# Performance work log

Hardware: AMD Instinct MI355X
Metric: run time of the kernel (lower is better)

## Reference

```python
import jax, jax.numpy as jnp
import numpy as np

N_NODES = 100000
N_EDGES = 1600000
IN_F = 128
HID = 128
N_ACT = 32
N_GRAPHS = 256


def setup_inputs() -> dict:
    key = jax.random.key(0)
    ks = jax.random.split(key, 8)
    x = jax.random.normal(ks[0], (N_NODES, IN_F), dtype=jnp.float32)
    edge_index = jax.random.randint(ks[1], (2, N_EDGES), 0, N_NODES, dtype=jnp.int64 if jax.config.read('jax_enable_x64') else jnp.int32)
    batch = jnp.sort(jax.random.randint(ks[2], (N_NODES,), 0, N_GRAPHS))
    def glorot(k, shape):
        fan_in = shape[0]
        return jax.random.normal(k, shape, dtype=jnp.float32) / jnp.sqrt(jnp.float32(fan_in))
    return {
        'x': x,
        'edge_index': edge_index,
        'batch': batch,
        'W1': glorot(ks[3], (IN_F, HID)), 'b1': jnp.zeros((HID,), jnp.float32),
        'W2': glorot(ks[4], (HID, HID)), 'b2': jnp.zeros((HID,), jnp.float32),
        'Wl1': glorot(ks[5], (HID, HID)), 'bl1': jnp.zeros((HID,), jnp.float32),
        'Wl2': glorot(ks[6], (HID, N_ACT)), 'bl2': jnp.zeros((N_ACT,), jnp.float32),
    }


def gcn_conv(x, src, dst, W, b, n_nodes):
    """PyG GCNConv: add self-loops, sym-normalize by deg^{-1/2} (deg counted at dst)."""
    h = x @ W  # [N, F_out]
    # degree including self-loop (computed on destination/col, per gcn_norm)
    deg = jax.ops.segment_sum(jnp.ones((src.shape[0],), h.dtype), dst,
                              num_segments=n_nodes) + 1.0
    dinv = jax.lax.rsqrt(deg)  # deg >= 1, no inf handling needed
    norm = dinv[src] * dinv[dst]  # [E]
    agg = jax.ops.segment_sum(norm[:, None] * h[src], dst, num_segments=n_nodes)
    # self-loop contribution: dinv[i]^2 * h[i]
    return agg + (dinv * dinv)[:, None] * h + b


def global_mean_pool(x, batch, num_graphs):
    s = jax.ops.segment_sum(x, batch, num_segments=num_graphs)
    cnt = jax.ops.segment_sum(jnp.ones((x.shape[0],), x.dtype), batch,
                              num_segments=num_graphs)
    return s / jnp.maximum(cnt, 1.0)[:, None]


def reference(x, edge_index, batch, W1, b1, W2, b2, Wl1, bl1, Wl2, bl2):
    src, dst = edge_index[0], edge_index[1]
    n = x.shape[0]
    h = jax.nn.relu(gcn_conv(x, src, dst, W1, b1, n))
    h = jax.nn.relu(gcn_conv(h, src, dst, W2, b2, n))
    g = global_mean_pool(h, batch, N_GRAPHS)  # [G, HID]
    g = jax.nn.relu(g @ Wl1 + bl1)
    return g @ Wl2 + bl2  # [G, N_ACT]
```

## Files before the change

### kernel.cpp

```cpp
#include <hip/hip_runtime.h>
#include <hip/hip_bf16.h>

#define N_NODES 100000
#define N_EDGES 1600000
#define NFEAT   128
#define NGRAPH  256
#define NACT    32
#define ECAP    64
#define OVF_CAP 8192

#define BUCK_SHIFT 9
#define BUCK_NODES 512
#define NBUCK ((N_NODES + BUCK_NODES - 1) / BUCK_NODES)
#define SEGCAP 10240
#define CHUNK 4096
#define NBLK1 ((N_EDGES + CHUNK - 1) / CHUNK)
#define BIN_NODES 128
#define NBLK2 ((N_NODES + BIN_NODES - 1) / BIN_NODES)
#define GB ((N_NODES + 63) / 64)
#define WTBLK (2 * NFEAT * NFEAT / 256)
#define LDSROW 136

typedef __attribute__((ext_vector_type(8))) short bf16x8;
typedef __attribute__((ext_vector_type(4))) float f32x4;

__device__ inline unsigned short f2bf(float f) {
  __hip_bfloat16 b = __float2bfloat16(f);
  return *reinterpret_cast<unsigned short*>(&b);
}
__device__ inline float2 bfu2f(unsigned u) {
  __hip_bfloat162 t = *reinterpret_cast<__hip_bfloat162*>(&u);
  return __bfloat1622float2(t);
}

__global__ __launch_bounds__(256) void edgepart_wt_kernel(const int* __restrict__ src,
                                                          const int* __restrict__ dst,
                                                          int* __restrict__ bucket_cursor,
                                                          int2* __restrict__ seg,
                                                          int* __restrict__ cnt,
                                                          int* __restrict__ ovf_cnt,
                                                          int* __restrict__ ovf,
                                                          const float* __restrict__ W1,
                                                          const float* __restrict__ W2,
                                                          unsigned short* __restrict__ Wt1,
                                                          unsigned short* __restrict__ Wt2) {
  __shared__ int2 stage[CHUNK];
  __shared__ int hist[NBUCK], offs[NBUCK], cursor[NBUCK], gbase[NBUCK];
  __shared__ int sc[256];
  int tid = threadIdx.x;

  if (blockIdx.x >= NBLK1) {
    int i = (blockIdx.x - NBLK1) * 256 + tid;
    int which = i >> 14;
    int idx = i & 16383;
    int n = idx >> 7, k = idx & 127;
    if (which == 0) Wt1[n * NFEAT + k] = f2bf(W1[k * NFEAT + n]);
    else            Wt2[n * NFEAT + k] = f2bf(W2[k * NFEAT + n]);
    return;
  }

  int e0 = blockIdx.x * CHUNK;
  int m = N_EDGES - e0; if (m > CHUNK) m = CHUNK;

  for (int i = tid; i < NBUCK; i += 256) hist[i] = 0;
  __syncthreads();

  for (int i = tid; i < m; i += 256)
    atomicAdd(&hist[dst[e0 + i] >> BUCK_SHIFT], 1);
  __syncthreads();

  sc[tid] = (tid < NBUCK) ? hist[tid] : 0;
  __syncthreads();
  for (int ofs = 1; ofs < 256; ofs <<= 1) {
    int t = (tid >= ofs) ? sc[tid - ofs] : 0;
    __syncthreads();
    sc[tid] += t;
    __syncthreads();
  }
  if (tid < NBUCK) {
    int o = tid ? sc[tid - 1] : 0;
    offs[tid] = o;
    cursor[tid] = o;
    gbase[tid] = hist[tid] ? atomicAdd(&bucket_cursor[tid], hist[tid]) : 0;
  }
  __syncthreads();

  for (int i = tid; i < m; i += 256) {
    int2 p = make_int2(src[e0 + i], dst[e0 + i]);
    int pos = atomicAdd(&cursor[p.y >> BUCK_SHIFT], 1);
    stage[pos] = p;
  }
  __syncthreads();

  for (int i = tid; i < m; i += 256) {
    int2 p = stage[i];
    int bd = p.y >> BUCK_SHIFT;
    int gpos = gbase[bd] + (i - offs[bd]);
    if (gpos < SEGCAP) {
      seg[(size_t)bd * SEGCAP + gpos] = p;
    } else {
      atomicAdd(&cnt[p.y], 1);
      int o = atomicAdd(ovf_cnt, 1);
      if (o < OVF_CAP) { ovf[2 * o] = p.x; ovf[2 * o + 1] = p.y; }
    }
  }
}

__global__ __launch_bounds__(256) void binbuild_gemm_kernel(const int2* __restrict__ seg,
                                                            const int* __restrict__ bucket_cursor,
                                                            int* __restrict__ cnt,
                                                            float* __restrict__ dinv,
                                                            int* __restrict__ elist,
                                                            int* __restrict__ ovf_cnt,
                                                            int* __restrict__ ovf,
                                                            const float* __restrict__ x,
                                                            const unsigned short* __restrict__ Wt,
                                                            unsigned short* __restrict__ C) {
  __shared__ int lcnt[BIN_NODES];
  __shared__ int lel[BIN_NODES * ECAP];
  int tid = threadIdx.x;

  if (blockIdx.x >= NBLK2) {
    int bid = blockIdx.x - NBLK2;
    int wave = tid >> 6, lane = tid & 63;
    int q = lane >> 4, r = lane & 15;
    int m0 = bid * 64 + wave * 16;
    int arow = m0 + r; if (arow > N_NODES - 1) arow = N_NODES - 1;
    const float* Arow = x + (size_t)arow * NFEAT;

    f32x4 acc[8];
    #pragma unroll
    for (int t = 0; t < 8; ++t) acc[t] = (f32x4){0.f, 0.f, 0.f, 0.f};

    #pragma unroll
    for (int s = 0; s < 4; ++s) {
      int k0 = s * 32 + q * 8;
      float4 a0 = *(const float4*)(Arow + k0);
      float4 a1 = *(const float4*)(Arow + k0 + 4);
      bf16x8 xf;
      xf[0] = (short)f2bf(a0.x); xf[1] = (short)f2bf(a0.y);
      xf[2] = (short)f2bf(a0.z); xf[3] = (short)f2bf(a0.w);
      xf[4] = (short)f2bf(a1.x); xf[5] = (short)f2bf(a1.y);
      xf[6] = (short)f2bf(a1.z); xf[7] = (short)f2bf(a1.w);
      #pragma unroll
      for (int t = 0; t < 8; ++t) {
        bf16x8 wf = *(const bf16x8*)(Wt + (size_t)(t * 16 + r) * NFEAT + k0);
        acc[t] = __builtin_amdgcn_mfma_f32_16x16x32_bf16(wf, xf, acc[t], 0, 0, 0);
      }
    }
    int node = m0 + r;
    if (node < N_NODES) {
      uint2* Crow = (uint2*)(C + (size_t)node * NFEAT);
      #pragma unroll
      for (int t = 0; t < 8; ++t) {
        uint2 v;
        v.x = ((unsigned)f2bf(acc[t][1]) << 16) | f2bf(acc[t][0]);
        v.y = ((unsigned)f2bf(acc[t][3]) << 16) | f2bf(acc[t][2]);
        Crow[t * 4 + q] = v;
      }
    }
    return;
  }

  int n0 = blockIdx.x * BIN_NODES;
  int pb = n0 >> BUCK_SHIFT;
  if (tid < BIN_NODES) lcnt[tid] = 0;
  __syncthreads();
  int m = bucket_cursor[pb]; if (m > SEGCAP) m = SEGCAP;
  const int2* s = seg + (size_t)pb * SEGCAP;
  for (int e = tid; e < m; e += 256) {
    int2 p = s[e];
    unsigned ln = (unsigned)(p.y - n0);
    if (ln < (unsigned)BIN_NODES) {
      int pos = atomicAdd(&lcnt[ln], 1);
      if (pos < ECAP) {
        lel[(ln << 6) + pos] = p.x;
      } else {
        int o = atomicAdd(ovf_cnt, 1);
        if (o < OVF_CAP) { ovf[2 * o] = p.x; ovf[2 * o + 1] = p.y; }
      }
    }
  }
  __syncthreads();
  if (tid < BIN_NODES) {
    int n = n0 + tid;
    if (n < N_NODES) {
      int tot = cnt[n] + lcnt[tid];
      cnt[n] = tot;
      dinv[n] = rsqrtf((float)tot + 1.0f);
    }
  }
  int4* gel = (int4*)(elist + (size_t)n0 * ECAP);
  const int4* lel4 = (const int4*)lel;
  for (int i = tid; i < BIN_NODES * ECAP / 4; i += 256) gel[i] = lel4[i];
}

__global__ __launch_bounds__(512) void agg_gemm_kernel(const uint2* __restrict__ h2,
                                                       const int* __restrict__ elist,
                                                       const int* __restrict__ cnt,
                                                       const float* __restrict__ dinv,
                                                       const float* __restrict__ bias,
                                                       const int* __restrict__ ovf_cnt,
                                                       const int* __restrict__ ovf,
                                                       const unsigned short* __restrict__ Wt2,
                                                       unsigned short* __restrict__ H2) {
  __shared__ __align__(16) unsigned short hloc[16 * LDSROW];
  int tid = threadIdx.x;
  int lane = tid & 63;
  int lw = tid >> 6;
  int hl = lane & 31;
  int n0 = blockIdx.x * 16;
  int nloc = lw * 2 + (lane >> 5);
  int n = n0 + nloc;

  float dn = dinv[n];
  int c = cnt[n]; c = (c > ECAP) ? ECAP : c;
  const int* el = elist + (size_t)n * ECAP;

  int   s0 = (hl < c)      ? el[hl]      : n;
  float w0 = (hl < c)      ? dinv[s0] * dn : 0.f;
  int   s1 = (hl + 32 < c) ? el[hl + 32] : n;
  float w1 = (hl + 32 < c) ? dinv[s1] * dn : 0.f;

  int cA = __shfl(c, 0), cB = __shfl(c, 32);
  int cmax = cA > cB ? cA : cB;

  uint2 hv = h2[(size_t)n * 32 + hl];
  float2 vlo = bfu2f(hv.x), vhi = bfu2f(hv.y);
  float sw = dn * dn;
  float a0 = sw * vlo.x, a1 = sw * vlo.y, a2 = sw * vhi.x, a3 = sw * vhi.y;

  int e1 = cmax < 32 ? cmax : 32;
  e1 = (e1 + 7) & ~7;
  for (int j = 0; j < e1; j += 8) {
    uint2 pv[8]; float w[8];
    #pragma unroll
    for (int u = 0; u < 8; ++u) {
      int s = __shfl(s0, j + u, 32);
      w[u] = __shfl(w0, j + u, 32);
      pv[u] = h2[(size_t)s * 32 + hl];
    }
    #pragma unroll
    for (int u = 0; u < 8; ++u) {
      float2 lo = bfu2f(pv[u].x), hi = bfu2f(pv[u].y);
      a0 = fmaf(w[u], lo.x, a0); a1 = fmaf(w[u], lo.y, a1);
      a2 = fmaf(w[u], hi.x, a2); a3 = fmaf(w[u], hi.y, a3);
    }
  }
  if (cmax > 32) {
    int e2 = ((cmax - 32) + 7) & ~7;
    for (int j = 0; j < e2; j += 8) {
      uint2 pv[8]; float w[8];
      #pragma unroll
      for (int u = 0; u < 8; ++u) {
        int s = __shfl(s1, j + u, 32);
        w[u] = __shfl(w1, j + u, 32);
        pv[u] = h2[(size_t)s * 32 + hl];
      }
      #pragma unroll
      for (int u = 0; u < 8; ++u) {
        float2 lo = bfu2f(pv[u].x), hi = bfu2f(pv[u].y);
        a0 = fmaf(w[u], lo.x, a0); a1 = fmaf(w[u], lo.y, a1);
        a2 = fmaf(w[u], hi.x, a2); a3 = fmaf(w[u], hi.y, a3);
      }
    }
  }

  int m = *ovf_cnt; if (m > OVF_CAP) m = OVF_CAP;
  for (int p = 0; p < m; ++p) {
    int s = ovf[2 * p], d = ovf[2 * p + 1];
    if (d == n) {
      float w = dinv[s] * dn;
      uint2 pv = h2[(size_t)s * 32 + hl];
      float2 lo = bfu2f(pv.x), hi = bfu2f(pv.y);
      a0 = fmaf(w, lo.x, a0); a1 = fmaf(w, lo.y, a1);
      a2 = fmaf(w, hi.x, a2); a3 = fmaf(w, hi.y, a3);
    }
  }

  float4 b4 = ((const float4*)bias)[hl];
  uint2 v;
  v.x = ((unsigned)f2bf(fmaxf(a1 + b4.y, 0.f)) << 16) | f2bf(fmaxf(a0 + b4.x, 0.f));
  v.y = ((unsigned)f2bf(fmaxf(a3 + b4.w, 0.f)) << 16) | f2bf(fmaxf(a2 + b4.z, 0.f));
  *(uint2*)(&hloc[nloc * LDSROW + hl * 4]) = v;
  __syncthreads();

  int q = lane >> 4, r = lane & 15;
  f32x4 acc = (f32x4){0.f, 0.f, 0.f, 0.f};
  #pragma unroll
  for (int s = 0; s < 4; ++s) {
    int k0 = s * 32 + q * 8;
    bf16x8 xf = *(const bf16x8*)(&hloc[r * LDSROW + k0]);
    bf16x8 wf = *(const bf16x8*)(Wt2 + (size_t)(lw * 16 + r) * NFEAT + k0);
    acc = __builtin_amdgcn_mfma_f32_16x16x32_bf16(wf, xf, acc, 0, 0, 0);
  }
  int node = n0 + r;
  uint2* Crow = (uint2*)(H2 + (size_t)node * NFEAT);
  uint2 o;
  o.x = ((unsigned)f2bf(acc[1]) << 16) | f2bf(acc[0]);
  o.y = ((unsigned)f2bf(acc[3]) << 16) | f2bf(acc[2]);
  Crow[lw * 4 + q] = o;
}

__global__ __launch_bounds__(256) void agg_pool_kernel(const uint2* __restrict__ h2,
                                                       const int* __restrict__ elist,
                                                       const int* __restrict__ cnt,
                                                       const float* __restrict__ dinv,
                                                       const float* __restrict__ bias,
                                                       const int* __restrict__ ovf_cnt,
                                                       const int* __restrict__ ovf,
                                                       const int* __restrict__ batch,
                                                       float* __restrict__ gsum) {
  __shared__ float lds[8][NFEAT];
  int tid = threadIdx.x;
  int wid = (blockIdx.x * 256 + tid) >> 6;
  int lane = tid & 63;
  int hl = lane & 31;
  int n = wid * 2 + (lane >> 5);
  int n0 = blockIdx.x * 8;

  float dn = dinv[n];
  int c = cnt[n]; c = (c > ECAP) ? ECAP : c;
  const int* el = elist + (size_t)n * ECAP;

  int   s0 = (hl < c)      ? el[hl]      : n;
  float w0 = (hl < c)      ? dinv[s0] * dn : 0.f;
  int   s1 = (hl + 32 < c) ? el[hl + 32] : n;
  float w1 = (hl + 32 < c) ? dinv[s1] * dn : 0.f;

  int cA = __shfl(c, 0), cB = __shfl(c, 32);
  int cmax = cA > cB ? cA : cB;

  uint2 hv = h2[(size_t)n * 32 + hl];
  float2 vlo = bfu2f(hv.x), vhi = bfu2f(hv.y);
  float sw = dn * dn;
  float a0 = sw * vlo.x, a1 = sw * vlo.y, a2 = sw * vhi.x, a3 = sw * vhi.y;

  int e1 = cmax < 32 ? cmax : 32;
  e1 = (e1 + 7) & ~7;
  for (int j = 0; j < e1; j += 8) {
    uint2 pv[8]; float w[8];
    #pragma unroll
    for (int u = 0; u < 8; ++u) {
      int s = __shfl(s0, j + u, 32);
      w[u] = __shfl(w0, j + u, 32);
      pv[u] = h2[(size_t)s * 32 + hl];
    }
    #pragma unroll
    for (int u = 0; u < 8; ++u) {
      float2 lo = bfu2f(pv[u].x), hi = bfu2f(pv[u].y);
      a0 = fmaf(w[u], lo.x, a0); a1 = fmaf(w[u], lo.y, a1);
      a2 = fmaf(w[u], hi.x, a2); a3 = fmaf(w[u], hi.y, a3);
    }
  }
  if (cmax > 32) {
    int e2 = ((cmax - 32) + 7) & ~7;
    for (int j = 0; j < e2; j += 8) {
      uint2 pv[8]; float w[8];
      #pragma unroll
      for (int u = 0; u < 8; ++u) {
        int s = __shfl(s1, j + u, 32);
        w[u] = __shfl(w1, j + u, 32);
        pv[u] = h2[(size_t)s * 32 + hl];
      }
      #pragma unroll
      for (int u = 0; u < 8; ++u) {
        float2 lo = bfu2f(pv[u].x), hi = bfu2f(pv[u].y);
        a0 = fmaf(w[u], lo.x, a0); a1 = fmaf(w[u], lo.y, a1);
        a2 = fmaf(w[u], hi.x, a2); a3 = fmaf(w[u], hi.y, a3);
      }
    }
  }

  int m = *ovf_cnt; if (m > OVF_CAP) m = OVF_CAP;
  for (int p = 0; p < m; ++p) {
    int s = ovf[2 * p], d = ovf[2 * p + 1];
    if (d == n) {
      float w = dinv[s] * dn;
      uint2 pv = h2[(size_t)s * 32 + hl];
      float2 lo = bfu2f(pv.x), hi = bfu2f(pv.y);
      a0 = fmaf(w, lo.x, a0); a1 = fmaf(w, lo.y, a1);
      a2 = fmaf(w, hi.x, a2); a3 = fmaf(w, hi.y, a3);
    }
  }

  float4 b4 = ((const float4*)bias)[hl];
  int nloc = n - n0;
  lds[nloc][hl * 4 + 0] = fmaxf(a0 + b4.x, 0.f);
  lds[nloc][hl * 4 + 1] = fmaxf(a1 + b4.y, 0.f);
  lds[nloc][hl * 4 + 2] = fmaxf(a2 + b4.z, 0.f);
  lds[nloc][hl * 4 + 3] = fmaxf(a3 + b4.w, 0.f);
  __syncthreads();

  if (tid < NFEAT) {
    float sum = 0.f;
    int cur = batch[n0];
    #pragma unroll
    for (int i = 0; i < 8; ++i) {
      int b = batch[n0 + i];
      if (b != cur) {
        atomicAdd(&gsum[cur * NFEAT + tid], sum);
        sum = 0.f; cur = b;
      }
      sum += lds[i][tid];
    }
    atomicAdd(&gsum[cur * NFEAT + tid], sum);
  }
}

__global__ __launch_bounds__(128) void mlp_kernel(const float* __restrict__ gsum,
                                                  const int* __restrict__ batch,
                                                  const float* __restrict__ Wl1,
                                                  const float* __restrict__ bl1,
                                                  const float* __restrict__ Wl2,
                                                  const float* __restrict__ bl2,
                                                  float* __restrict__ out) {
  __shared__ float gr[NFEAT];
  __shared__ float t1[NFEAT];
  __shared__ float sinv;
  int g = blockIdx.x, t = threadIdx.x;
  if (t == 0) {
    int lo = 0, hi = N_NODES;
    while (lo < hi) { int mid = (lo + hi) >> 1; if (batch[mid] < g) lo = mid + 1; else hi = mid; }
    int lo2 = lo, hi2 = N_NODES;
    while (lo2 < hi2) { int mid = (lo2 + hi2) >> 1; if (batch[mid] < g + 1) lo2 = mid + 1; else hi2 = mid; }
    sinv = 1.0f / fmaxf((float)(lo2 - lo), 1.0f);
  }
  __syncthreads();
  gr[t] = gsum[g * NFEAT + t] * sinv;
  __syncthreads();
  float acc = bl1[t];
  for (int k = 0; k < NFEAT; ++k) acc = fmaf(gr[k], Wl1[k * NFEAT + t], acc);
  t1[t] = fmaxf(acc, 0.f);
  __syncthreads();
  if (t < NACT) {
    float a2 = bl2[t];
    for (int k = 0; k < NFEAT; ++k) a2 = fmaf(t1[k], Wl2[k * NACT + t], a2);
    out[g * NACT + t] = a2;
  }
}

extern "C" void kernel_launch(void* const* d_in, const int* in_sizes, int n_in,
                              void* d_out, int out_size, void* d_ws, size_t ws_size,
                              hipStream_t stream) {
  const float* x    = (const float*)d_in[0];
  const int*   ei   = (const int*)d_in[1];
  const int*   batch= (const int*)d_in[2];
  const float* W1   = (const float*)d_in[3];
  const float* b1   = (const float*)d_in[4];
  const float* W2   = (const float*)d_in[5];
  const float* b2   = (const float*)d_in[6];
  const float* Wl1  = (const float*)d_in[7];
  const float* bl1  = (const float*)d_in[8];
  const float* Wl2  = (const float*)d_in[9];
  const float* bl2  = (const float*)d_in[10];
  float* out = (float*)d_out;

  const int* srcp = ei;
  const int* dstp = ei + N_EDGES;

  char* base = (char*)d_ws;
  size_t off = 0;
  auto alloc = [&](size_t bytes) -> void* {
    void* p = base + off;
    off += (bytes + 511) & ~(size_t)511;
    return p;
  };
  int*   cnt     = (int*)alloc((size_t)N_NODES * 4);
  int*   ovfc    = (int*)alloc(4);
  float* gsum    = (float*)alloc((size_t)NGRAPH * NFEAT * 4);
  int*   bucket_cursor = (int*)alloc((size_t)NBUCK * 4);
  size_t zspan   = off;
  float* dinv    = (float*)alloc((size_t)N_NODES * 4);
  int*   elist   = (int*)alloc((size_t)NBLK2 * BIN_NODES * ECAP * 4);
  int*   ovf     = (int*)alloc((size_t)OVF_CAP * 2 * 4);
  int2*  seg     = (int2*)alloc((size_t)NBUCK * SEGCAP * 8);
  unsigned short* Wt1 = (unsigned short*)alloc((size_t)NFEAT * NFEAT * 2);
  unsigned short* Wt2 = (unsigned short*)alloc((size_t)NFEAT * NFEAT * 2);
  unsigned short* H1 = (unsigned short*)alloc((size_t)N_NODES * NFEAT * 2);
  unsigned short* H2 = (unsigned short*)alloc((size_t)N_NODES * NFEAT * 2);

  hipMemsetAsync(d_ws, 0, zspan, stream);

  const int AB = (N_NODES + 7) / 8;
  const int FB = N_NODES / 16;

  edgepart_wt_kernel<<<NBLK1 + WTBLK, 256, 0, stream>>>(
      srcp, dstp, bucket_cursor, seg, cnt, ovfc, ovf, W1, W2, Wt1, Wt2);
  binbuild_gemm_kernel<<<NBLK2 + GB, 256, 0, stream>>>(
      seg, bucket_cursor, cnt, dinv, elist, ovfc, ovf, x, Wt1, H1);
  agg_gemm_kernel<<<FB, 512, 0, stream>>>((const uint2*)H1, elist, cnt, dinv, b1,
                                          ovfc, ovf, Wt2, H2);
  agg_pool_kernel<<<AB, 256, 0, stream>>>((const uint2*)H2, elist, cnt, dinv, b2,
                                          ovfc, ovf, batch, gsum);
  mlp_kernel<<<NGRAPH, 128, 0, stream>>>(gsum, batch, Wl1, bl1, Wl2, bl2, out);
}
```

Baseline: 321.5 us.

## Gather one node per wavefront with 16-byte loads across four neighbor groups

Both aggregation kernels now give each node a full wavefront. Four 16-lane groups each fetch a different neighbor's 256-byte row with 16-byte loads, and the partial sums are combined with xor shuffles. This aims to put more independent gather loads in flight, use wider memory transactions, and remove the cost of pairing two nodes of different degree in one wavefront. The price is a cross-lane reduction, and in agg_gemm the 16-row MFMA tile now holds only 8 valid nodes. That doubles the MFMA work and weight loads per node.

```diff
diff --git a/kernel.cpp b/kernel.cpp
--- a/kernel.cpp
+++ b/kernel.cpp
@@ -208,60 +208,71 @@
   int tid = threadIdx.x;
   int lane = tid & 63;
   int lw = tid >> 6;
-  int hl = lane & 31;
-  int n0 = blockIdx.x * 16;
-  int nloc = lw * 2 + (lane >> 5);
-  int n = n0 + nloc;
+  int l16 = lane & 15;
+  int rg = lane >> 4;
+  int l32 = lane & 31;
+  int n0 = blockIdx.x * 8;
+  int n = n0 + lw;
 
   float dn = dinv[n];
   int c = cnt[n]; c = (c > ECAP) ? ECAP : c;
   const int* el = elist + (size_t)n * ECAP;
 
-  int   s0 = (hl < c)      ? el[hl]      : n;
-  float w0 = (hl < c)      ? dinv[s0] * dn : 0.f;
-  int   s1 = (hl + 32 < c) ? el[hl + 32] : n;
-  float w1 = (hl + 32 < c) ? dinv[s1] * dn : 0.f;
-
-  int cA = __shfl(c, 0), cB = __shfl(c, 32);
-  int cmax = cA > cB ? cA : cB;
-
-  uint2 hv = h2[(size_t)n * 32 + hl];
-  float2 vlo = bfu2f(hv.x), vhi = bfu2f(hv.y);
-  float sw = dn * dn;
-  float a0 = sw * vlo.x, a1 = sw * vlo.y, a2 = sw * vhi.x, a3 = sw * vhi.y;
-
-  int e1 = cmax < 32 ? cmax : 32;
-  e1 = (e1 + 7) & ~7;
-  for (int j = 0; j < e1; j += 8) {
-    uint2 pv[8]; float w[8];
-    #pragma unroll
-    for (int u = 0; u < 8; ++u) {
-      int s = __shfl(s0, j + u, 32);
-      w[u] = __shfl(w0, j + u, 32);
-      pv[u] = h2[(size_t)s * 32 + hl];
-    }
-    #pragma unroll
-    for (int u = 0; u < 8; ++u) {
-      float2 lo = bfu2f(pv[u].x), hi = bfu2f(pv[u].y);
-      a0 = fmaf(w[u], lo.x, a0); a1 = fmaf(w[u], lo.y, a1);
-      a2 = fmaf(w[u], hi.x, a2); a3 = fmaf(w[u], hi.y, a3);
-    }
-  }
-  if (cmax > 32) {
-    int e2 = ((cmax - 32) + 7) & ~7;
-    for (int j = 0; j < e2; j += 8) {
-      uint2 pv[8]; float w[8];
-      #pragma unroll
-      for (int u = 0; u < 8; ++u) {
-        int s = __shfl(s1, j + u, 32);
-        w[u] = __shfl(w1, j + u, 32);
-        pv[u] = h2[(size_t)s * 32 + hl];
-      }
-      #pragma unroll
-      for (int u = 0; u < 8; ++u) {
-        float2 lo = bfu2f(pv[u].x), hi = bfu2f(pv[u].y);
-        a0 = fmaf(w[u], lo.x, a0); a1 = fmaf(w[u], lo.y, a1);
-        a2 = fmaf(w[u], hi.x, a2); a3 = fmaf(w[u], hi.y, a3);
+  int   s0 = (l32 < c)      ? el[l32]      : n;
+  float w0 = (l32 < c)      ? dinv[s0] * dn : 0.f;
+  int   s1 = (l32 + 32 < c) ? el[l32 + 32] : n;
+  float w1 = (l32 + 32 < c) ? dinv[s1] * dn : 0.f;
+
+  const uint4* h4 = (const uint4*)h2;
+  uint4 hv = h4[(size_t)n * 16 + l16];
+  float sw = (rg == 0) ? dn * dn : 0.f;
+  float acc[8];
+  {
+    float2 f0 = bfu2f(hv.x), f1 = bfu2f(hv.y), f2 = bfu2f(hv.z), f3 = bfu2f(hv.w);
+    acc[0] = sw * f0.x; acc[1] = sw * f0.y; acc[2] = sw * f1.x; acc[3] = sw * f1.y;
+    acc[4] = sw * f2.x; acc[5] = sw * f2.y; acc[6] = sw * f3.x; acc[7] = sw * f3.y;
+  }
+
+  uint4 pv[8];
+  #pragma unroll
+  for (int r = 0; r < 8; ++r) pv[r] = hv;
+  #pragma unroll
+  for (int r = 0; r < 8; ++r) {
+    if (r * 4 < c) {
+      int s = __shfl(s0, r * 4 + rg, 32);
+      pv[r] = h4[(size_t)s * 16 + l16];
+    }
+  }
+  #pragma unroll
+  for (int r = 0; r < 8; ++r) {
+    if (r * 4 < c) {
+      float w = __shfl(w0, r * 4 + rg, 32);
+      float2 f0 = bfu2f(pv[r].x), f1 = bfu2f(pv[r].y);
+      float2 f2 = bfu2f(pv[r].z), f3 = bfu2f(pv[r].w);
+      acc[0] = fmaf(w, f0.x, acc[0]); acc[1] = fmaf(w, f0.y, acc[1]);
+      acc[2] = fmaf(w, f1.x, acc[2]); acc[3] = fmaf(w, f1.y, acc[3]);
+      acc[4] = fmaf(w, f2.x, acc[4]); acc[5] = fmaf(w, f2.y, acc[5]);
+      acc[6] = fmaf(w, f3.x, acc[6]); acc[7] = fmaf(w, f3.y, acc[7]);
+    }
+  }
+  if (c > 32) {
+    #pragma unroll
+    for (int r = 0; r < 8; ++r) {
+      if (32 + r * 4 < c) {
+        int s = __shfl(s1, r * 4 + rg, 32);
+        pv[r] = h4[(size_t)s * 16 + l16];
+      }
+    }
+    #pragma unroll
+    for (int r = 0; r < 8; ++r) {
+      if (32 + r * 4 < c) {
+        float w = __shfl(w1, r * 4 + rg, 32);
+        float2 f0 = bfu2f(pv[r].x), f1 = bfu2f(pv[r].y);
+        float2 f2 = bfu2f(pv[r].z), f3 = bfu2f(pv[r].w);
+        acc[0] = fmaf(w, f0.x, acc[0]); acc[1] = fmaf(w, f0.y, acc[1]);
+        acc[2] = fmaf(w, f1.x, acc[2]); acc[3] = fmaf(w, f1.y, acc[3]);
+        acc[4] = fmaf(w, f2.x, acc[4]); acc[5] = fmaf(w, f2.y, acc[5]);
+        acc[6] = fmaf(w, f3.x, acc[6]); acc[7] = fmaf(w, f3.y, acc[7]);
       }
     }
   }
@@ -270,39 +281,55 @@
   for (int p = 0; p < m; ++p) {
     int s = ovf[2 * p], d = ovf[2 * p + 1];
     if (d == n) {
-      float w = dinv[s] * dn;
-      uint2 pv = h2[(size_t)s * 32 + hl];
-      float2 lo = bfu2f(pv.x), hi = bfu2f(pv.y);
-      a0 = fmaf(w, lo.x, a0); a1 = fmaf(w, lo.y, a1);
-      a2 = fmaf(w, hi.x, a2); a3 = fmaf(w, hi.y, a3);
-    }
-  }
-
-  float4 b4 = ((const float4*)bias)[hl];
-  uint2 v;
-  v.x = ((unsigned)f2bf(fmaxf(a1 + b4.y, 0.f)) << 16) | f2bf(fmaxf(a0 + b4.x, 0.f));
-  v.y = ((unsigned)f2bf(fmaxf(a3 + b4.w, 0.f)) << 16) | f2bf(fmaxf(a2 + b4.z, 0.f));
-  *(uint2*)(&hloc[nloc * LDSROW + hl * 4]) = v;
+      float w = (rg == 0) ? dinv[s] * dn : 0.f;
+      uint4 pvv = h4[(size_t)s * 16 + l16];
+      float2 f0 = bfu2f(pvv.x), f1 = bfu2f(pvv.y);
+      float2 f2 = bfu2f(pvv.z), f3 = bfu2f(pvv.w);
+      acc[0] = fmaf(w, f0.x, acc[0]); acc[1] = fmaf(w, f0.y, acc[1]);
+      acc[2] = fmaf(w, f1.x, acc[2]); acc[3] = fmaf(w, f1.y, acc[3]);
+      acc[4] = fmaf(w, f2.x, acc[4]); acc[5] = fmaf(w, f2.y, acc[5]);
+      acc[6] = fmaf(w, f3.x, acc[6]); acc[7] = fmaf(w, f3.y, acc[7]);
+    }
+  }
+
+  #pragma unroll
+  for (int k = 0; k < 8; ++k) {
+    acc[k] += __shfl_xor(acc[k], 16);
+    acc[k] += __shfl_xor(acc[k], 32);
+  }
+
+  if (rg == 0) {
+    float4 b0 = ((const float4*)bias)[l16 * 2];
+    float4 b1 = ((const float4*)bias)[l16 * 2 + 1];
+    uint4 v;
+    v.x = ((unsigned)f2bf(fmaxf(acc[1] + b0.y, 0.f)) << 16) | f2bf(fmaxf(acc[0] + b0.x, 0.f));
+    v.y = ((unsigned)f2bf(fmaxf(acc[3] + b0.w, 0.f)) << 16) | f2bf(fmaxf(acc[2] + b0.z, 0.f));
+    v.z = ((unsigned)f2bf(fmaxf(acc[5] + b1.y, 0.f)) << 16) | f2bf(fmaxf(acc[4] + b1.x, 0.f));
+    v.w = ((unsigned)f2bf(fmaxf(acc[7] + b1.w, 0.f)) << 16) | f2bf(fmaxf(acc[6] + b1.z, 0.f));
+    *(uint4*)(&hloc[lw * LDSROW + l16 * 8]) = v;
+  }
   __syncthreads();
 
   int q = lane >> 4, r = lane & 15;
-  f32x4 acc = (f32x4){0.f, 0.f, 0.f, 0.f};
+  f32x4 acc2 = (f32x4){0.f, 0.f, 0.f, 0.f};
   #pragma unroll
   for (int s = 0; s < 4; ++s) {
     int k0 = s * 32 + q * 8;
     bf16x8 xf = *(const bf16x8*)(&hloc[r * LDSROW + k0]);
     bf16x8 wf = *(const bf16x8*)(Wt2 + (size_t)(lw * 16 + r) * NFEAT + k0);
-    acc = __builtin_amdgcn_mfma_f32_16x16x32_bf16(wf, xf, acc, 0, 0, 0);
-  }
-  int node = n0 + r;
-  uint2* Crow = (uint2*)(H2 + (size_t)node * NFEAT);
-  uint2 o;
-  o.x = ((unsigned)f2bf(acc[1]) << 16) | f2bf(acc[0]);
-  o.y = ((unsigned)f2bf(acc[3]) << 16) | f2bf(acc[2]);
-  Crow[lw * 4 + q] = o;
-}
-
-__global__ __launch_bounds__(256) void agg_pool_kernel(const uint2* __restrict__ h2,
+    acc2 = __builtin_amdgcn_mfma_f32_16x16x32_bf16(wf, xf, acc2, 0, 0, 0);
+  }
+  if (r < 8) {
+    int node = n0 + r;
+    uint2* Crow = (uint2*)(H2 + (size_t)node * NFEAT);
+    uint2 o;
+    o.x = ((unsigned)f2bf(acc2[1]) << 16) | f2bf(acc2[0]);
+    o.y = ((unsigned)f2bf(acc2[3]) << 16) | f2bf(acc2[2]);
+    Crow[lw * 4 + q] = o;
+  }
+}
+
+__global__ __launch_bounds__(512) void agg_pool_kernel(const uint2* __restrict__ h2,
                                                        const int* __restrict__ elist,
                                                        const int* __restrict__ cnt,
                                                        const float* __restrict__ dinv,
@@ -313,61 +340,73 @@
                                                        float* __restrict__ gsum) {
   __shared__ float lds[8][NFEAT];
   int tid = threadIdx.x;
-  int wid = (blockIdx.x * 256 + tid) >> 6;
   int lane = tid & 63;
-  int hl = lane & 31;
-  int n = wid * 2 + (lane >> 5);
+  int lw = tid >> 6;
+  int l16 = lane & 15;
+  int rg = lane >> 4;
+  int l32 = lane & 31;
   int n0 = blockIdx.x * 8;
+  int n = n0 + lw;
 
   float dn = dinv[n];
   int c = cnt[n]; c = (c > ECAP) ? ECAP : c;
   const int* el = elist + (size_t)n * ECAP;
 
-  int   s0 = (hl < c)      ? el[hl]      : n;
-  float w0 = (hl < c)      ? dinv[s0] * dn : 0.f;
-  int   s1 = (hl + 32 < c) ? el[hl + 32] : n;
-  float w1 = (hl + 32 < c) ? dinv[s1] * dn : 0.f;
-
-  int cA = __shfl(c, 0), cB = __shfl(c, 32);
-  int cmax = cA > cB ? cA : cB;
-
-  uint2 hv = h2[(size_t)n * 32 + hl];
-  float2 vlo = bfu2f(hv.x), vhi = bfu2f(hv.y);
-  float sw = dn * dn;
-  float a0 = sw * vlo.x, a1 = sw * vlo.y, a2 = sw * vhi.x, a3 = sw * vhi.y;
-
-  int e1 = cmax < 32 ? cmax : 32;
-  e1 = (e1 + 7) & ~7;
-  for (int j = 0; j < e1; j += 8) {
-    uint2 pv[8]; float w[8];
-    #pragma unroll
-    for (int u = 0; u < 8; ++u) {
-      int s = __shfl(s0, j + u, 32);
-      w[u] = __shfl(w0, j + u, 32);
-      pv[u] = h2[(size_t)s * 32 + hl];
-    }
-    #pragma unroll
-    for (int u = 0; u < 8; ++u) {
-      float2 lo = bfu2f(pv[u].x), hi = bfu2f(pv[u].y);
-      a0 = fmaf(w[u], lo.x, a0); a1 = fmaf(w[u], lo.y, a1);
-      a2 = fmaf(w[u], hi.x, a2); a3 = fmaf(w[u], hi.y, a3);
-    }
-  }
-  if (cmax > 32) {
-    int e2 = ((cmax - 32) + 7) & ~7;
-    for (int j = 0; j < e2; j += 8) {
-      uint2 pv[8]; float w[8];
-      #pragma unroll
-      for (int u = 0; u < 8; ++u) {
-        int s = __shfl(s1, j + u, 32);
-        w[u] = __shfl(w1, j + u, 32);
-        pv[u] = h2[(size_t)s * 32 + hl];
-      }
-      #pragma unroll
-      for (int u = 0; u < 8; ++u) {
-        float2 lo = bfu2f(pv[u].x), hi = bfu2f(pv[u].y);
-        a0 = fmaf(w[u], lo.x, a0); a1 = fmaf(w[u], lo.y, a1);
-        a2 = fmaf(w[u], hi.x, a2); a3 = fmaf(w[u], hi.y, a3);
+  int   s0 = (l32 < c)      ? el[l32]      : n;
+  float w0 = (l32 < c)      ? dinv[s0] * dn : 0.f;
+  int   s1 = (l32 + 32 < c) ? el[l32 + 32] : n;
+  float w1 = (l32 + 32 < c) ? dinv[s1] * dn : 0.f;
+
+  const uint4* h4 = (const uint4*)h2;
+  uint4 hv = h4[(size_t)n * 16 + l16];
+  float sw = (rg == 0) ? dn * dn : 0.f;
+  float acc[8];
+  {
+    float2 f0 = bfu2f(hv.x), f1 = bfu2f(hv.y), f2 = bfu2f(hv.z), f3 = bfu2f(hv.w);
+    acc[0] = sw * f0.x; acc[1] = sw * f0.y; acc[2] = sw * f1.x; acc[3] = sw * f1.y;
+    acc[4] = sw * f2.x; acc[5] = sw * f2.y; acc[6] = sw * f3.x; acc[7] = sw * f3.y;
+  }
+
+  uint4 pv[8];
+  #pragma unroll
+  for (int r = 0; r < 8; ++r) pv[r] = hv;
+  #pragma unroll
+  for (int r = 0; r < 8; ++r) {
+    if (r * 4 < c) {
+      int s = __shfl(s0, r * 4 + rg, 32);
+      pv[r] = h4[(size_t)s * 16 + l16];
+    }
+  }
+  #pragma unroll
+  for (int r = 0; r < 8; ++r) {
+    if (r * 4 < c) {
+      float w = __shfl(w0, r * 4 + rg, 32);
+      float2 f0 = bfu2f(pv[r].x), f1 = bfu2f(pv[r].y);
+      float2 f2 = bfu2f(pv[r].z), f3 = bfu2f(pv[r].w);
+      acc[0] = fmaf(w, f0.x, acc[0]); acc[1] = fmaf(w, f0.y, acc[1]);
+      acc[2] = fmaf(w, f1.x, acc[2]); acc[3] = fmaf(w, f1.y, acc[3]);
+      acc[4] = fmaf(w, f2.x, acc[4]); acc[5] = fmaf(w, f2.y, acc[5]);
+      acc[6] = fmaf(w, f3.x, acc[6]); acc[7] = fmaf(w, f3.y, acc[7]);
+    }
+  }
+  if (c > 32) {
+    #pragma unroll
+    for (int r = 0; r < 8; ++r) {
+      if (32 + r * 4 < c) {
+        int s = __shfl(s1, r * 4 + rg, 32);
+        pv[r] = h4[(size_t)s * 16 + l16];
+      }
+    }
+    #pragma unroll
+    for (int r = 0; r < 8; ++r) {
+      if (32 + r * 4 < c) {
+        float w = __shfl(w1, r * 4 + rg, 32);
+        float2 f0 = bfu2f(pv[r].x), f1 = bfu2f(pv[r].y);
+        float2 f2 = bfu2f(pv[r].z), f3 = bfu2f(pv[r].w);
+        acc[0] = fmaf(w, f0.x, acc[0]); acc[1] = fmaf(w, f0.y, acc[1]);
+        acc[2] = fmaf(w, f1.x, acc[2]); acc[3] = fmaf(w, f1.y, acc[3]);
+        acc[4] = fmaf(w, f2.x, acc[4]); acc[5] = fmaf(w, f2.y, acc[5]);
+        acc[6] = fmaf(w, f3.x, acc[6]); acc[7] = fmaf(w, f3.y, acc[7]);
       }
     }
   }
@@ -376,20 +415,34 @@
   for (int p = 0; p < m; ++p) {
     int s = ovf[2 * p], d = ovf[2 * p + 1];
     if (d == n) {
-      float w = dinv[s] * dn;
-      uint2 pv = h2[(size_t)s * 32 + hl];
-      float2 lo = bfu2f(pv.x), hi = bfu2f(pv.y);
-      a0 = fmaf(w, lo.x, a0); a1 = fmaf(w, lo.y, a1);
-      a2 = fmaf(w, hi.x, a2); a3 = fmaf(w, hi.y, a3);
-    }
-  }
-
-  float4 b4 = ((const float4*)bias)[hl];
-  int nloc = n - n0;
-  lds[nloc][hl * 4 + 0] = fmaxf(a0 + b4.x, 0.f);
-  lds[nloc][hl * 4 + 1] = fmaxf(a1 + b4.y, 0.f);
-  lds[nloc][hl * 4 + 2] = fmaxf(a2 + b4.z, 0.f);
-  lds[nloc][hl * 4 + 3] = fmaxf(a3 + b4.w, 0.f);
+      float w = (rg == 0) ? dinv[s] * dn : 0.f;
+      uint4 pvv = h4[(size_t)s * 16 + l16];
+      float2 f0 = bfu2f(pvv.x), f1 = bfu2f(pvv.y);
+      float2 f2 = bfu2f(pvv.z), f3 = bfu2f(pvv.w);
+      acc[0] = fmaf(w, f0.x, acc[0]); acc[1] = fmaf(w, f0.y, acc[1]);
+      acc[2] = fmaf(w, f1.x, acc[2]); acc[3] = fmaf(w, f1.y, acc[3]);
+      acc[4] = fmaf(w, f2.x, acc[4]); acc[5] = fmaf(w, f2.y, acc[5]);
+      acc[6] = fmaf(w, f3.x, acc[6]); acc[7] = fmaf(w, f3.y, acc[7]);
+    }
+  }
+
+  #pragma unroll
+  for (int k = 0; k < 8; ++k) {
+    acc[k] += __shfl_xor(acc[k], 16);
+    acc[k] += __shfl_xor(acc[k], 32);
+  }
+
+  if (rg == 0) {
+    float4 b0 = ((const float4*)bias)[l16 * 2];
+    float4 b1 = ((const float4*)bias)[l16 * 2 + 1];
+    float4 v0, v1;
+    v0.x = fmaxf(acc[0] + b0.x, 0.f); v0.y = fmaxf(acc[1] + b0.y, 0.f);
+    v0.z = fmaxf(acc[2] + b0.z, 0.f); v0.w = fmaxf(acc[3] + b0.w, 0.f);
+    v1.x = fmaxf(acc[4] + b1.x, 0.f); v1.y = fmaxf(acc[5] + b1.y, 0.f);
+    v1.z = fmaxf(acc[6] + b1.z, 0.f); v1.w = fmaxf(acc[7] + b1.w, 0.f);
+    *(float4*)(&lds[lw][l16 * 8]) = v0;
+    *(float4*)(&lds[lw][l16 * 8 + 4]) = v1;
+  }
   __syncthreads();
 
   if (tid < NFEAT) {
@@ -482,8 +535,7 @@
 
   hipMemsetAsync(d_ws, 0, zspan, stream);
 
-  const int AB = (N_NODES + 7) / 8;
-  const int FB = N_NODES / 16;
+  const int FB = N_NODES / 8;
 
   edgepart_wt_kernel<<<NBLK1 + WTBLK, 256, 0, stream>>>(
       srcp, dstp, bucket_cursor, seg, cnt, ovfc, ovf, W1, W2, Wt1, Wt2);
@@ -491,7 +543,7 @@
       seg, bucket_cursor, cnt, dinv, elist, ovfc, ovf, x, Wt1, H1);
   agg_gemm_kernel<<<FB, 512, 0, stream>>>((const uint2*)H1, elist, cnt, dinv, b1,
                                           ovfc, ovf, Wt2, H2);
-  agg_pool_kernel<<<AB, 256, 0, stream>>>((const uint2*)H2, elist, cnt, dinv, b2,
+  agg_pool_kernel<<<FB, 512, 0, stream>>>((const uint2*)H2, elist, cnt, dinv, b2,
                                           ovfc, ovf, batch, gsum);
   mlp_kernel<<<NGRAPH, 128, 0, stream>>>(gsum, batch, Wl1, bl1, Wl2, bl2, out);
 }
```

Result: slower. 341.5 us (+6.2%).

## Pre-scale GEMM outputs by dinv and count degrees during partitioning

Applied to the files above, without the earlier changes.

Degrees are now counted with global atomics in the first partition pass, so the GEMM epilogue can compute dinv itself and store h already scaled by dinv[src]. The aggregation loops then sum the gathered rows without per-edge weight lookups or shuffles, and apply dinv[dst] once in the epilogue. This removes the dependent dinv[s] gathers and the weight shuffles from the edge loop. The cost is 1.6M global atomics on cnt in the partition kernel, plus extra bf16 rounding from storing pre-scaled values.

```diff
diff --git a/kernel.cpp b/kernel.cpp
--- a/kernel.cpp
+++ b/kernel.cpp
@@ -65,8 +65,11 @@
   for (int i = tid; i < NBUCK; i += 256) hist[i] = 0;
   __syncthreads();
 
-  for (int i = tid; i < m; i += 256)
-    atomicAdd(&hist[dst[e0 + i] >> BUCK_SHIFT], 1);
+  for (int i = tid; i < m; i += 256) {
+    int d = dst[e0 + i];
+    atomicAdd(&hist[d >> BUCK_SHIFT], 1);
+    atomicAdd(&cnt[d], 1);
+  }
   __syncthreads();
 
   sc[tid] = (tid < NBUCK) ? hist[tid] : 0;
@@ -99,7 +102,6 @@
     if (gpos < SEGCAP) {
       seg[(size_t)bd * SEGCAP + gpos] = p;
     } else {
-      atomicAdd(&cnt[p.y], 1);
       int o = atomicAdd(ovf_cnt, 1);
       if (o < OVF_CAP) { ovf[2 * o] = p.x; ovf[2 * o + 1] = p.y; }
     }
@@ -108,7 +110,7 @@
 
 __global__ __launch_bounds__(256) void binbuild_gemm_kernel(const int2* __restrict__ seg,
                                                             const int* __restrict__ bucket_cursor,
-                                                            int* __restrict__ cnt,
+                                                            const int* __restrict__ cnt,
                                                             float* __restrict__ dinv,
                                                             int* __restrict__ elist,
                                                             int* __restrict__ ovf_cnt,
@@ -150,12 +152,13 @@
     }
     int node = m0 + r;
     if (node < N_NODES) {
+      float dv = rsqrtf((float)cnt[node] + 1.0f);
       uint2* Crow = (uint2*)(C + (size_t)node * NFEAT);
       #pragma unroll
       for (int t = 0; t < 8; ++t) {
         uint2 v;
-        v.x = ((unsigned)f2bf(acc[t][1]) << 16) | f2bf(acc[t][0]);
-        v.y = ((unsigned)f2bf(acc[t][3]) << 16) | f2bf(acc[t][2]);
+        v.x = ((unsigned)f2bf(dv * acc[t][1]) << 16) | f2bf(dv * acc[t][0]);
+        v.y = ((unsigned)f2bf(dv * acc[t][3]) << 16) | f2bf(dv * acc[t][2]);
         Crow[t * 4 + q] = v;
       }
     }
@@ -184,11 +187,8 @@
   __syncthreads();
   if (tid < BIN_NODES) {
     int n = n0 + tid;
-    if (n < N_NODES) {
-      int tot = cnt[n] + lcnt[tid];
-      cnt[n] = tot;
-      dinv[n] = rsqrtf((float)tot + 1.0f);
-    }
+    if (n < N_NODES)
+      dinv[n] = rsqrtf((float)cnt[n] + 1.0f);
   }
   int4* gel = (int4*)(elist + (size_t)n0 * ECAP);
   const int4* lel4 = (const int4*)lel;
@@ -217,51 +217,48 @@
   int c = cnt[n]; c = (c > ECAP) ? ECAP : c;
   const int* el = elist + (size_t)n * ECAP;
 
-  int   s0 = (hl < c)      ? el[hl]      : n;
-  float w0 = (hl < c)      ? dinv[s0] * dn : 0.f;
-  int   s1 = (hl + 32 < c) ? el[hl + 32] : n;
-  float w1 = (hl + 32 < c) ? dinv[s1] * dn : 0.f;
+  int s0 = (hl < c)      ? el[hl]      : n;
+  int s1 = (hl + 32 < c) ? el[hl + 32] : n;
 
   int cA = __shfl(c, 0), cB = __shfl(c, 32);
   int cmax = cA > cB ? cA : cB;
 
   uint2 hv = h2[(size_t)n * 32 + hl];
   float2 vlo = bfu2f(hv.x), vhi = bfu2f(hv.y);
-  float sw = dn * dn;
-  float a0 = sw * vlo.x, a1 = sw * vlo.y, a2 = sw * vhi.x, a3 = sw * vhi.y;
+  float a0 = vlo.x, a1 = vlo.y, a2 = vhi.x, a3 = vhi.y;
 
   int e1 = cmax < 32 ? cmax : 32;
   e1 = (e1 + 7) & ~7;
   for (int j = 0; j < e1; j += 8) {
-    uint2 pv[8]; float w[8];
+    uint2 pv[8];
     #pragma unroll
     for (int u = 0; u < 8; ++u) {
       int s = __shfl(s0, j + u, 32);
-      w[u] = __shfl(w0, j + u, 32);
       pv[u] = h2[(size_t)s * 32 + hl];
     }
     #pragma unroll
     for (int u = 0; u < 8; ++u) {
-      float2 lo = bfu2f(pv[u].x), hi = bfu2f(pv[u].y);
-      a0 = fmaf(w[u], lo.x, a0); a1 = fmaf(w[u], lo.y, a1);
-      a2 = fmaf(w[u], hi.x, a2); a3 = fmaf(w[u], hi.y, a3);
+      if (j + u < c) {
+        float2 lo = bfu2f(pv[u].x), hi = bfu2f(pv[u].y);
+        a0 += lo.x; a1 += lo.y; a2 += hi.x; a3 += hi.y;
+      }
     }
   }
   if (cmax > 32) {
-    int e2 = ((cmax - 32) + 7) & ~7;
-    for (int j = 0; j < e2; j += 8) {
-      uint2 pv[8]; float w[8];
+    int e2 = 32 + (((cmax - 32) + 7) & ~7);
+    for (int j = 32; j < e2; j += 8) {
+      uint2 pv[8];
       #pragma unroll
       for (int u = 0; u < 8; ++u) {
-        int s = __shfl(s1, j + u, 32);
-        w[u] = __shfl(w1, j + u, 32);
+        int s = __shfl(s1, j - 32 + u, 32);
         pv[u] = h2[(size_t)s * 32 + hl];
       }
       #pragma unroll
       for (int u = 0; u < 8; ++u) {
-        float2 lo = bfu2f(pv[u].x), hi = bfu2f(pv[u].y);
-        a0 = fmaf(w[u], lo.x, a0); a1 = fmaf(w[u], lo.y, a1);
-        a2 = fmaf(w[u], hi.x, a2); a3 = fmaf(w[u], hi.y, a3);
+        if (j + u < c) {
+          float2 lo = bfu2f(pv[u].x), hi = bfu2f(pv[u].y);
+          a0 += lo.x; a1 += lo.y; a2 += hi.x; a3 += hi.y;
+        }
       }
     }
   }
@@ -270,18 +267,18 @@
   for (int p = 0; p < m; ++p) {
     int s = ovf[2 * p], d = ovf[2 * p + 1];
     if (d == n) {
-      float w = dinv[s] * dn;
       uint2 pv = h2[(size_t)s * 32 + hl];
       float2 lo = bfu2f(pv.x), hi = bfu2f(pv.y);
-      a0 = fmaf(w, lo.x, a0); a1 = fmaf(w, lo.y, a1);
-      a2 = fmaf(w, hi.x, a2); a3 = fmaf(w, hi.y, a3);
+      a0 += lo.x; a1 += lo.y; a2 += hi.x; a3 += hi.y;
     }
   }
 
   float4 b4 = ((const float4*)bias)[hl];
   uint2 v;
-  v.x = ((unsigned)f2bf(fmaxf(a1 + b4.y, 0.f)) << 16) | f2bf(fmaxf(a0 + b4.x, 0.f));
-  v.y = ((unsigned)f2bf(fmaxf(a3 + b4.w, 0.f)) << 16) | f2bf(fmaxf(a2 + b4.z, 0.f));
+  v.x = ((unsigned)f2bf(fmaxf(fmaf(dn, a1, b4.y), 0.f)) << 16) |
+        f2bf(fmaxf(fmaf(dn, a0, b4.x), 0.f));
+  v.y = ((unsigned)f2bf(fmaxf(fmaf(dn, a3, b4.w), 0.f)) << 16) |
+        f2bf(fmaxf(fmaf(dn, a2, b4.z), 0.f));
   *(uint2*)(&hloc[nloc * LDSROW + hl * 4]) = v;
   __syncthreads();
 
@@ -295,10 +292,11 @@
     acc = __builtin_amdgcn_mfma_f32_16x16x32_bf16(wf, xf, acc, 0, 0, 0);
   }
   int node = n0 + r;
+  float dvr = dinv[node];
   uint2* Crow = (uint2*)(H2 + (size_t)node * NFEAT);
   uint2 o;
-  o.x = ((unsigned)f2bf(acc[1]) << 16) | f2bf(acc[0]);
-  o.y = ((unsigned)f2bf(acc[3]) << 16) | f2bf(acc[2]);
+  o.x = ((unsigned)f2bf(dvr * acc[1]) << 16) | f2bf(dvr * acc[0]);
+  o.y = ((unsigned)f2bf(dvr * acc[3]) << 16) | f2bf(dvr * acc[2]);
   Crow[lw * 4 + q] = o;
 }
 
@@ -323,51 +321,48 @@
   int c = cnt[n]; c = (c > ECAP) ? ECAP : c;
   const int* el = elist + (size_t)n * ECAP;
 
-  int   s0 = (hl < c)      ? el[hl]      : n;
-  float w0 = (hl < c)      ? dinv[s0] * dn : 0.f;
-  int   s1 = (hl + 32 < c) ? el[hl + 32] : n;
-  float w1 = (hl + 32 < c) ? dinv[s1] * dn : 0.f;
+  int s0 = (hl < c)      ? el[hl]      : n;
+  int s1 = (hl + 32 < c) ? el[hl + 32] : n;
 
   int cA = __shfl(c, 0), cB = __shfl(c, 32);
   int cmax = cA > cB ? cA : cB;
 
   uint2 hv = h2[(size_t)n * 32 + hl];
   float2 vlo = bfu2f(hv.x), vhi = bfu2f(hv.y);
-  float sw = dn * dn;
-  float a0 = sw * vlo.x, a1 = sw * vlo.y, a2 = sw * vhi.x, a3 = sw * vhi.y;
+  float a0 = vlo.x, a1 = vlo.y, a2 = vhi.x, a3 = vhi.y;
 
   int e1 = cmax < 32 ? cmax : 32;
   e1 = (e1 + 7) & ~7;
   for (int j = 0; j < e1; j += 8) {
-    uint2 pv[8]; float w[8];
+    uint2 pv[8];
     #pragma unroll
     for (int u = 0; u < 8; ++u) {
       int s = __shfl(s0, j + u, 32);
-      w[u] = __shfl(w0, j + u, 32);
       pv[u] = h2[(size_t)s * 32 + hl];
     }
     #pragma unroll
     for (int u = 0; u < 8; ++u) {
-      float2 lo = bfu2f(pv[u].x), hi = bfu2f(pv[u].y);
-      a0 = fmaf(w[u], lo.x, a0); a1 = fmaf(w[u], lo.y, a1);
-      a2 = fmaf(w[u], hi.x, a2); a3 = fmaf(w[u], hi.y, a3);
+      if (j + u < c) {
+        float2 lo = bfu2f(pv[u].x), hi = bfu2f(pv[u].y);
+        a0 += lo.x; a1 += lo.y; a2 += hi.x; a3 += hi.y;
+      }
     }
   }
   if (cmax > 32) {
-    int e2 = ((cmax - 32) + 7) & ~7;
-    for (int j = 0; j < e2; j += 8) {
-      uint2 pv[8]; float w[8];
+    int e2 = 32 + (((cmax - 32) + 7) & ~7);
+    for (int j = 32; j < e2; j += 8) {
+      uint2 pv[8];
       #pragma unroll
       for (int u = 0; u < 8; ++u) {
-        int s = __shfl(s1, j + u, 32);
-        w[u] = __shfl(w1, j + u, 32);
+        int s = __shfl(s1, j - 32 + u, 32);
         pv[u] = h2[(size_t)s * 32 + hl];
       }
       #pragma unroll
       for (int u = 0; u < 8; ++u) {
-        float2 lo = bfu2f(pv[u].x), hi = bfu2f(pv[u].y);
-        a0 = fmaf(w[u], lo.x, a0); a1 = fmaf(w[u], lo.y, a1);
-        a2 = fmaf(w[u], hi.x, a2); a3 = fmaf(w[u], hi.y, a3);
+        if (j + u < c) {
+          float2 lo = bfu2f(pv[u].x), hi = bfu2f(pv[u].y);
+          a0 += lo.x; a1 += lo.y; a2 += hi.x; a3 += hi.y;
+        }
       }
     }
   }
@@ -376,20 +371,18 @@
   for (int p = 0; p < m; ++p) {
     int s = ovf[2 * p], d = ovf[2 * p + 1];
     if (d == n) {
-      float w = dinv[s] * dn;
       uint2 pv = h2[(size_t)s * 32 + hl];
       float2 lo = bfu2f(pv.x), hi = bfu2f(pv.y);
-      a0 = fmaf(w, lo.x, a0); a1 = fmaf(w, lo.y, a1);
-      a2 = fmaf(w, hi.x, a2); a3 = fmaf(w, hi.y, a3);
+      a0 += lo.x; a1 += lo.y; a2 += hi.x; a3 += hi.y;
     }
   }
 
   float4 b4 = ((const float4*)bias)[hl];
   int nloc = n - n0;
-  lds[nloc][hl * 4 + 0] = fmaxf(a0 + b4.x, 0.f);
-  lds[nloc][hl * 4 + 1] = fmaxf(a1 + b4.y, 0.f);
-  lds[nloc][hl * 4 + 2] = fmaxf(a2 + b4.z, 0.f);
-  lds[nloc][hl * 4 + 3] = fmaxf(a3 + b4.w, 0.f);
+  lds[nloc][hl * 4 + 0] = fmaxf(fmaf(dn, a0, b4.x), 0.f);
+  lds[nloc][hl * 4 + 1] = fmaxf(fmaf(dn, a1, b4.y), 0.f);
+  lds[nloc][hl * 4 + 2] = fmaxf(fmaf(dn, a2, b4.z), 0.f);
+  lds[nloc][hl * 4 + 3] = fmaxf(fmaf(dn, a3, b4.w), 0.f);
   __syncthreads();
 
   if (tid < NFEAT) {
```

Result: slower. 365.5 us (+13.7%).
